# Kernel optimization log

Measured on AMD Instinct MI355X. Metric: run time of the kernel, lower is better.

The kernel has to match this reference:

```python
import jax, jax.numpy as jnp
import numpy as np

B, A, F, T = 4096, 64, 124, 8
H1, H2 = 64, 16


def setup_inputs() -> dict:
    key = jax.random.key(0)
    ks = jax.random.split(key, 10)
    x = jax.random.normal(ks[0], (B, A, F + 1), dtype=jnp.float32)
    types = jax.random.randint(ks[1], (B, A), 0, T).astype(jnp.float32)
    x = x.at[:, :, 0].set(types)  # column 0 stores atom-type index
    mask = (jax.random.uniform(ks[2], (B, A)) < 0.9).astype(jnp.float32)
    s1 = 1.0 / np.sqrt(F)
    s2 = 1.0 / np.sqrt(H1)
    s3 = 1.0 / np.sqrt(H2)
    return {
        "x_padded": x,
        "mask": mask,
        "W1": jax.random.normal(ks[3], (T, F, H1), dtype=jnp.float32) * s1,
        "b1": jax.random.normal(ks[4], (T, H1), dtype=jnp.float32) * s1,
        "W2": jax.random.normal(ks[5], (T, H1, H2), dtype=jnp.float32) * s2,
        "b2": jax.random.normal(ks[6], (T, H2), dtype=jnp.float32) * s2,
        "W3": jax.random.normal(ks[7], (T, H2, 1), dtype=jnp.float32) * s3,
        "b3": jax.random.normal(ks[8], (T, 1), dtype=jnp.float32) * s3,
    }


def reference(x_padded, mask, W1, b1, W2, b2, W3, b3):
    # x_padded: [B, A, 1+F]; mask: [B, A]
    type_idx = x_padded[:, :, 0].astype(jnp.int32)           # [B, A]
    feats = x_padded[:, :, 1:]                               # [B, A, F]
    n_types = W1.shape[0]
    # Faithful to the original: every type's subnet runs on the FULL batch
    # with non-matching atoms zero-masked (bias paths still contribute).
    type_mask = (type_idx[None, :, :] == jnp.arange(n_types)[:, None, None]).astype(feats.dtype)  # [T,B,A]
    sel = feats[None, :, :, :] * type_mask[..., None]        # [T,B,A,F]
    h = jax.nn.relu(jnp.einsum('tbaf,tfh->tbah', sel, W1) + b1[:, None, None, :])
    h = jax.nn.relu(jnp.einsum('tbah,thg->tbag', h, W2) + b2[:, None, None, :])
    o = jnp.einsum('tbag,tgo->tbao', h, W3) + b3[:, None, None, :]  # [T,B,A,1]
    per_atom = (o[..., 0] * mask[None, :, :]).sum(axis=0)   # [B, A]
    return per_atom.sum(axis=1, keepdims=True)               # [B, 1]
```

## Files before the change

kernel.cpp:

```cpp
#include <hip/hip_runtime.h>
#include <stdint.h>

#define NMOL 4096
#define NATOMS (NMOL * 64)
#define NF 124
#define NT 8
#define ROWV 125

#define WS_DCONST  0
#define WS_TOTALS  64
#define WS_CURSOR  96
#define WS_HIST    128
#define WS_W1S     8320
#define WS_W2T     139392
#define WS_TYPEBUF 155776
#define WS_LIST    417920

#define HS 72

typedef __attribute__((ext_vector_type(8))) short short8;
typedef __attribute__((ext_vector_type(4))) float floatx4;
typedef __attribute__((ext_vector_type(4), aligned(4))) float floatx4u;
typedef __attribute__((ext_vector_type(4))) unsigned int uint4v;

__device__ __forceinline__ unsigned short f2bf(float f) {
    unsigned u = __builtin_bit_cast(unsigned, f);
    u += 0x7fffu + ((u >> 16) & 1u);
    return (unsigned short)(u >> 16);
}
__device__ __forceinline__ unsigned pk2(float a, float b) {
    return (unsigned)f2bf(a) | ((unsigned)f2bf(b) << 16);
}
__device__ __forceinline__ void ld_lds16(const void* g, void* lds) {
    __builtin_amdgcn_global_load_lds(
        (const __attribute__((address_space(1))) unsigned int*)g,
        (__attribute__((address_space(3))) unsigned int*)lds, 16, 0, 0);
}

__global__ __launch_bounds__(256) void k_hist(const float* __restrict__ x,
                                              const float* __restrict__ mask,
                                              unsigned* __restrict__ hist256,
                                              unsigned char* __restrict__ typebuf,
                                              float* __restrict__ out) {
    __shared__ unsigned hist[NT];
    int tid = threadIdx.x, b = blockIdx.x;
    if (tid < NT) hist[tid] = 0u;
    __syncthreads();
    int base = b * 1024;
    for (int i = 0; i < 4; ++i) {
        int atom = base + i * 256 + tid;
        float tf = x[(size_t)atom * ROWV];
        float m  = mask[atom];
        unsigned char tb = 0xFF;
        if (m != 0.0f) { tb = (unsigned char)(int)tf; atomicAdd(&hist[tb], 1u); }
        typebuf[atom] = tb;
    }
    if (b < 16) out[b * 256 + tid] = 0.0f;
    __syncthreads();
    if (tid < NT) hist256[b * NT + tid] = hist[tid];
}

__global__ __launch_bounds__(256) void k_setup(const float* __restrict__ W1,
                                               const float* __restrict__ b1,
                                               const float* __restrict__ W2,
                                               const float* __restrict__ b2,
                                               const float* __restrict__ W3,
                                               const float* __restrict__ b3,
                                               const unsigned* __restrict__ hist256,
                                               float* __restrict__ dconst,
                                               unsigned* __restrict__ totals,
                                               unsigned* __restrict__ cursor,
                                               unsigned short* __restrict__ W1S,
                                               unsigned short* __restrict__ W2T) {
    int tid = threadIdx.x, b = blockIdx.x;
    if (b == 0) {
        __shared__ float c[NT];
        __shared__ unsigned part[16][NT];
        __shared__ unsigned tot[NT];
        if (tid < 128) {
            int t = tid >> 4, g = tid & 15;
            float acc = b2[t * 16 + g];
            for (int h = 0; h < 64; ++h) {
                float h1 = b1[t * 64 + h];
                h1 = h1 > 0.f ? h1 : 0.f;
                acc += h1 * W2[(size_t)t * 1024 + h * 16 + g];
            }
            float h2 = acc > 0.f ? acc : 0.f;
            float v = h2 * W3[t * 16 + g];
            #pragma unroll
            for (int off = 1; off < 16; off <<= 1) v += __shfl_xor(v, off);
            if (g == 0) c[t] = v + b3[t];
        }
        if (tid < 128) {
            int t = tid & 7, chunk = tid >> 3;
            unsigned s = 0;
            for (int j = 0; j < 16; ++j) s += hist256[(chunk * 16 + j) * NT + t];
            part[chunk][t] = s;
        }
        __syncthreads();
        if (tid < NT) {
            unsigned s = 0;
            for (int j = 0; j < 16; ++j) s += part[j][tid];
            tot[tid] = s;
            totals[tid] = s;
        }
        __syncthreads();
        if (tid == 0) {
            float T_ = 0.f;
            for (int i = 0; i < NT; ++i) T_ += c[i];
            unsigned run = 0;
            for (int i = 0; i < NT; ++i) {
                dconst[i] = T_ - c[i] + b3[i];
                cursor[i] = run;
                run += tot[i];
            }
        }
    } else {
        int t = b - 1;
        const float* w1g = W1 + (size_t)t * NF * 64;
        unsigned short* dst = W1S + (size_t)t * 8192;
        for (int id = tid; id < 1024; id += 256) {
            int h = id >> 4, cc = id & 15;
            unsigned u[4];
            #pragma unroll
            for (int j = 0; j < 4; ++j) {
                int f0 = cc * 8 + 2 * j;
                unsigned short lo = (f0 < NF)     ? f2bf(w1g[f0 * 64 + h])       : (unsigned short)0;
                unsigned short hi = (f0 + 1 < NF) ? f2bf(w1g[(f0 + 1) * 64 + h]) : (unsigned short)0;
                u[j] = (unsigned)lo | ((unsigned)hi << 16);
            }
            int p = cc ^ (h & 15);
            *(uint4v*)(dst + h * 128 + p * 8) = (uint4v){u[0], u[1], u[2], u[3]};
        }
        unsigned short* d2 = W2T + (size_t)t * 1024;
        for (int i = tid; i < 1024; i += 256) {
            int g = i >> 6, h = i & 63;
            d2[i] = f2bf(W2[(size_t)t * 1024 + h * 16 + g]);
        }
    }
}

__global__ __launch_bounds__(256) void k_scatter(const unsigned char* __restrict__ typebuf,
                                                 unsigned* cursor, unsigned* list) {
    __shared__ unsigned hist[NT], basep[NT], cur[NT];
    int tid = threadIdx.x;
    if (tid < NT) { hist[tid] = 0u; cur[tid] = 0u; }
    __syncthreads();
    int base = blockIdx.x * 1024;
    unsigned char tb[4];
    for (int i = 0; i < 4; ++i) {
        tb[i] = typebuf[base + i * 256 + tid];
        if (tb[i] != 0xFF) atomicAdd(&hist[tb[i]], 1u);
    }
    __syncthreads();
    if (tid < NT && hist[tid]) basep[tid] = atomicAdd(&cursor[tid], hist[tid]);
    __syncthreads();
    for (int i = 0; i < 4; ++i) {
        if (tb[i] != 0xFF) {
            unsigned p = basep[tb[i]] + atomicAdd(&cur[tb[i]], 1u);
            list[p] = (unsigned)(base + i * 256 + tid);
        }
    }
}

__global__ __launch_bounds__(256, 4) void k_mlp(const float* __restrict__ x,
                                                const unsigned short* __restrict__ W1S,
                                                const float* __restrict__ b1,
                                                const unsigned short* __restrict__ W2T,
                                                const float* __restrict__ b2,
                                                const float* __restrict__ W3,
                                                const unsigned* __restrict__ totals,
                                                const float* __restrict__ dconst,
                                                const unsigned* __restrict__ list,
                                                float* __restrict__ out) {
    __shared__ unsigned short sW[64 * 128];
    __shared__ unsigned short sH[128 * HS];
    __shared__ unsigned sIds[128];

    unsigned g = blockIdx.x;
    unsigned cnt[NT], st[NT];
    {
        unsigned s = 0;
        for (int i = 0; i < NT; ++i) { cnt[i] = totals[i]; st[i] = s; s += cnt[i]; }
    }
    int t = -1; unsigned tile = 0;
    {
        unsigned tl = 0;
        for (int i = 0; i < NT; ++i) {
            unsigned nt_ = (cnt[i] + 127u) >> 7;
            if (t < 0 && g < tl + nt_) { t = i; tile = g - tl; }
            tl += nt_;
        }
    }
    if (t < 0) return;

    int valid = (int)cnt[t] - (int)(tile << 7);
    if (valid > 128) valid = 128;
    unsigned rowstart = st[t] + (tile << 7);

    int tid  = threadIdx.x;
    int wv   = tid >> 6;
    int lane = tid & 63;
    int quad = lane >> 4, l15 = lane & 15;
    int rowbase = wv * 32;

    {
        const char* src = (const char*)W1S + (size_t)t * 16384 + wv * 4096 + lane * 16;
        char*       dst = (char*)sW + wv * 4096;
        #pragma unroll
        for (int i = 0; i < 4; ++i) ld_lds16(src + i * 1024, dst + i * 1024);
    }
    if (tid < 128) sIds[tid] = list[rowstart + (tid < valid ? tid : 0)];

    float b1v[4];
    #pragma unroll
    for (int n = 0; n < 4; ++n) b1v[n] = b1[t * 64 + n * 16 + l15];

    __syncthreads();

    short8 afrag[2][4];
    #pragma unroll
    for (int m = 0; m < 2; ++m) {
        unsigned atom = sIds[rowbase + m * 16 + l15];
        const float* rp = x + (size_t)atom * ROWV + 1;
        #pragma unroll
        for (int ks = 0; ks < 4; ++ks) {
            int k0 = ks * 32 + quad * 8;
            floatx4 f0 = (floatx4)(*(const floatx4u*)(rp + k0));
            floatx4 f1 = (floatx4)0.f;
            if (!(ks == 3 && quad == 3))
                f1 = (floatx4)(*(const floatx4u*)(rp + k0 + 4));
            uint4v uu = (uint4v){pk2(f0[0], f0[1]), pk2(f0[2], f0[3]),
                                 pk2(f1[0], f1[1]), pk2(f1[2], f1[3])};
            afrag[m][ks] = __builtin_bit_cast(short8, uu);
        }
    }

    floatx4 c1[2][4];
    #pragma unroll
    for (int m = 0; m < 2; ++m)
        #pragma unroll
        for (int n = 0; n < 4; ++n) c1[m][n] = (floatx4)0.f;

    #pragma unroll
    for (int ks = 0; ks < 4; ++ks) {
        short8 bf[4];
        #pragma unroll
        for (int n = 0; n < 4; ++n)
            bf[n] = *(const short8*)(sW + (n * 16 + l15) * 128 + (((ks * 4 + quad) ^ l15) << 3));
        #pragma unroll
        for (int n = 0; n < 4; ++n) {
            c1[0][n] = __builtin_amdgcn_mfma_f32_16x16x32_bf16(afrag[0][ks], bf[n], c1[0][n], 0, 0, 0);
            c1[1][n] = __builtin_amdgcn_mfma_f32_16x16x32_bf16(afrag[1][ks], bf[n], c1[1][n], 0, 0, 0);
        }
    }

    #pragma unroll
    for (int m = 0; m < 2; ++m)
        #pragma unroll
        for (int n = 0; n < 4; ++n) {
            int col = n * 16 + l15;
            #pragma unroll
            for (int r = 0; r < 4; ++r) {
                float v = c1[m][n][r] + b1v[n];
                v = v > 0.f ? v : 0.f;
                sH[(rowbase + m * 16 + quad * 4 + r) * HS + col] = f2bf(v);
            }
        }

    const unsigned short* w2t = W2T + (size_t)t * 1024;
    floatx4 c2[2];
    c2[0] = (floatx4)0.f; c2[1] = (floatx4)0.f;
    #pragma unroll
    for (int ks = 0; ks < 2; ++ks) {
        int ko = ks * 32 + quad * 8;
        short8 a0 = *(const short8*)(sH + (rowbase + l15) * HS + ko);
        short8 a1 = *(const short8*)(sH + (rowbase + 16 + l15) * HS + ko);
        short8 bw = *(const short8*)(w2t + l15 * 64 + ko);
        c2[0] = __builtin_amdgcn_mfma_f32_16x16x32_bf16(a0, bw, c2[0], 0, 0, 0);
        c2[1] = __builtin_amdgcn_mfma_f32_16x16x32_bf16(a1, bw, c2[1], 0, 0, 0);
    }

    float b2v = b2[t * 16 + l15];
    float w3v = W3[t * 16 + l15];
    float dct = dconst[t];
    #pragma unroll
    for (int m = 0; m < 2; ++m) {
        float h2v[4];
        #pragma unroll
        for (int r = 0; r < 4; ++r) {
            float v = c2[m][r] + b2v;
            v = v > 0.f ? v : 0.f;
            h2v[r] = v * w3v;
        }
        #pragma unroll
        for (int off = 1; off < 16; off <<= 1)
            #pragma unroll
            for (int r = 0; r < 4; ++r) h2v[r] += __shfl_xor(h2v[r], off);
        if (l15 == 0) {
            #pragma unroll
            for (int r = 0; r < 4; ++r) {
                int row = rowbase + m * 16 + quad * 4 + r;
                if (row < valid) {
                    unsigned atom = sIds[row];
                    atomicAdd(&out[atom >> 6], h2v[r] + dct);
                }
            }
        }
    }
}

extern "C" void kernel_launch(void* const* d_in, const int* in_sizes, int n_in,
                              void* d_out, int out_size, void* d_ws, size_t ws_size,
                              hipStream_t stream) {
    const float* x    = (const float*)d_in[0];
    const float* mask = (const float*)d_in[1];
    const float* W1   = (const float*)d_in[2];
    const float* b1   = (const float*)d_in[3];
    const float* W2   = (const float*)d_in[4];
    const float* b2   = (const float*)d_in[5];
    const float* W3   = (const float*)d_in[6];
    const float* b3   = (const float*)d_in[7];
    float* out = (float*)d_out;

    char* ws = (char*)d_ws;
    float*          dconst  = (float*)(ws + WS_DCONST);
    unsigned*       totals  = (unsigned*)(ws + WS_TOTALS);
    unsigned*       cursor  = (unsigned*)(ws + WS_CURSOR);
    unsigned*       hist256 = (unsigned*)(ws + WS_HIST);
    unsigned short* W1S     = (unsigned short*)(ws + WS_W1S);
    unsigned short* W2T     = (unsigned short*)(ws + WS_W2T);
    unsigned char*  typebuf = (unsigned char*)(ws + WS_TYPEBUF);
    unsigned*       list    = (unsigned*)(ws + WS_LIST);

    k_hist<<<256, 256, 0, stream>>>(x, mask, hist256, typebuf, out);
    k_setup<<<9, 256, 0, stream>>>(W1, b1, W2, b2, W3, b3, hist256,
                                   dconst, totals, cursor, W1S, W2T);
    k_scatter<<<256, 256, 0, stream>>>(typebuf, cursor, list);
    k_mlp<<<2055, 256, 0, stream>>>(x, W1S, b1, W2T, b2, W3,
                                    totals, dconst, list, out);
}
```

Baseline: 224.7 us.

## Replace histogram+prefix pass with fixed-capacity per-type buckets, dropping a kernel

Removes the separate histogram kernel and the global prefix sum by giving each atom type a fixed-capacity bucket of 65536 slots. The sort kernel reads types and mask directly and atomically appends into each type's bucket. The MLP grid becomes a fixed 8x512 blocks, and each block derives its type and tile from its index and exits early if empty. Output zeroing moves into the setup kernel. This saves one launch and one pass over the type column, at the cost of launching many empty MLP blocks and assuming no type exceeds the capacity.

After: 217.3 us. 1.03x faster.

```diff
diff --git a/kernel.cpp b/kernel.cpp
--- a/kernel.cpp
+++ b/kernel.cpp
@@ -6,15 +6,13 @@
 #define NF 124
 #define NT 8
 #define ROWV 125
+#define CAP 65536
 
 #define WS_DCONST  0
-#define WS_TOTALS  64
-#define WS_CURSOR  96
-#define WS_HIST    128
-#define WS_W1S     8320
-#define WS_W2T     139392
-#define WS_TYPEBUF 155776
-#define WS_LIST    417920
+#define WS_CURSOR  64
+#define WS_W1S     128
+#define WS_W2T     131200
+#define WS_LIST    147712
 
 #define HS 72
 
@@ -35,29 +33,6 @@
     __builtin_amdgcn_global_load_lds(
         (const __attribute__((address_space(1))) unsigned int*)g,
         (__attribute__((address_space(3))) unsigned int*)lds, 16, 0, 0);
-}
-
-__global__ __launch_bounds__(256) void k_hist(const float* __restrict__ x,
-                                              const float* __restrict__ mask,
-                                              unsigned* __restrict__ hist256,
-                                              unsigned char* __restrict__ typebuf,
-                                              float* __restrict__ out) {
-    __shared__ unsigned hist[NT];
-    int tid = threadIdx.x, b = blockIdx.x;
-    if (tid < NT) hist[tid] = 0u;
-    __syncthreads();
-    int base = b * 1024;
-    for (int i = 0; i < 4; ++i) {
-        int atom = base + i * 256 + tid;
-        float tf = x[(size_t)atom * ROWV];
-        float m  = mask[atom];
-        unsigned char tb = 0xFF;
-        if (m != 0.0f) { tb = (unsigned char)(int)tf; atomicAdd(&hist[tb], 1u); }
-        typebuf[atom] = tb;
-    }
-    if (b < 16) out[b * 256 + tid] = 0.0f;
-    __syncthreads();
-    if (tid < NT) hist256[b * NT + tid] = hist[tid];
 }
 
 __global__ __launch_bounds__(256) void k_setup(const float* __restrict__ W1,
@@ -66,17 +41,14 @@
                                                const float* __restrict__ b2,
                                                const float* __restrict__ W3,
                                                const float* __restrict__ b3,
-                                               const unsigned* __restrict__ hist256,
                                                float* __restrict__ dconst,
-                                               unsigned* __restrict__ totals,
                                                unsigned* __restrict__ cursor,
                                                unsigned short* __restrict__ W1S,
-                                               unsigned short* __restrict__ W2T) {
+                                               unsigned short* __restrict__ W2T,
+                                               float* __restrict__ out) {
     int tid = threadIdx.x, b = blockIdx.x;
     if (b == 0) {
         __shared__ float c[NT];
-        __shared__ unsigned part[16][NT];
-        __shared__ unsigned tot[NT];
         if (tid < 128) {
             int t = tid >> 4, g = tid & 15;
             float acc = b2[t * 16 + g];
@@ -91,31 +63,14 @@
             for (int off = 1; off < 16; off <<= 1) v += __shfl_xor(v, off);
             if (g == 0) c[t] = v + b3[t];
         }
-        if (tid < 128) {
-            int t = tid & 7, chunk = tid >> 3;
-            unsigned s = 0;
-            for (int j = 0; j < 16; ++j) s += hist256[(chunk * 16 + j) * NT + t];
-            part[chunk][t] = s;
-        }
-        __syncthreads();
-        if (tid < NT) {
-            unsigned s = 0;
-            for (int j = 0; j < 16; ++j) s += part[j][tid];
-            tot[tid] = s;
-            totals[tid] = s;
-        }
+        if (tid < NT) cursor[tid] = (unsigned)(tid * CAP);
         __syncthreads();
         if (tid == 0) {
             float T_ = 0.f;
             for (int i = 0; i < NT; ++i) T_ += c[i];
-            unsigned run = 0;
-            for (int i = 0; i < NT; ++i) {
-                dconst[i] = T_ - c[i] + b3[i];
-                cursor[i] = run;
-                run += tot[i];
-            }
-        }
-    } else {
+            for (int i = 0; i < NT; ++i) dconst[i] = T_ - c[i] + b3[i];
+        }
+    } else if (b <= 8) {
         int t = b - 1;
         const float* w1g = W1 + (size_t)t * NF * 64;
         unsigned short* dst = W1S + (size_t)t * 8192;
@@ -137,11 +92,15 @@
             int g = i >> 6, h = i & 63;
             d2[i] = f2bf(W2[(size_t)t * 1024 + h * 16 + g]);
         }
-    }
-}
-
-__global__ __launch_bounds__(256) void k_scatter(const unsigned char* __restrict__ typebuf,
-                                                 unsigned* cursor, unsigned* list) {
+    } else {
+        out[(b - 9) * 256 + tid] = 0.0f;
+    }
+}
+
+__global__ __launch_bounds__(256) void k_sort(const float* __restrict__ x,
+                                              const float* __restrict__ mask,
+                                              unsigned* __restrict__ cursor,
+                                              unsigned* __restrict__ list) {
     __shared__ unsigned hist[NT], basep[NT], cur[NT];
     int tid = threadIdx.x;
     if (tid < NT) { hist[tid] = 0u; cur[tid] = 0u; }
@@ -149,8 +108,11 @@
     int base = blockIdx.x * 1024;
     unsigned char tb[4];
     for (int i = 0; i < 4; ++i) {
-        tb[i] = typebuf[base + i * 256 + tid];
-        if (tb[i] != 0xFF) atomicAdd(&hist[tb[i]], 1u);
+        int atom = base + i * 256 + tid;
+        float tf = x[(size_t)atom * ROWV];
+        float m  = mask[atom];
+        tb[i] = 0xFF;
+        if (m != 0.0f) { tb[i] = (unsigned char)(int)tf; atomicAdd(&hist[tb[i]], 1u); }
     }
     __syncthreads();
     if (tid < NT && hist[tid]) basep[tid] = atomicAdd(&cursor[tid], hist[tid]);
@@ -169,7 +131,7 @@
                                                 const unsigned short* __restrict__ W2T,
                                                 const float* __restrict__ b2,
                                                 const float* __restrict__ W3,
-                                                const unsigned* __restrict__ totals,
+                                                const unsigned* __restrict__ cursor,
                                                 const float* __restrict__ dconst,
                                                 const unsigned* __restrict__ list,
                                                 float* __restrict__ out) {
@@ -177,26 +139,13 @@
     __shared__ unsigned short sH[128 * HS];
     __shared__ unsigned sIds[128];
 
-    unsigned g = blockIdx.x;
-    unsigned cnt[NT], st[NT];
-    {
-        unsigned s = 0;
-        for (int i = 0; i < NT; ++i) { cnt[i] = totals[i]; st[i] = s; s += cnt[i]; }
-    }
-    int t = -1; unsigned tile = 0;
-    {
-        unsigned tl = 0;
-        for (int i = 0; i < NT; ++i) {
-            unsigned nt_ = (cnt[i] + 127u) >> 7;
-            if (t < 0 && g < tl + nt_) { t = i; tile = g - tl; }
-            tl += nt_;
-        }
-    }
-    if (t < 0) return;
-
-    int valid = (int)cnt[t] - (int)(tile << 7);
+    int t    = blockIdx.x >> 9;
+    int tile = blockIdx.x & 511;
+    int cnt  = (int)(cursor[t] - (unsigned)(t * CAP));
+    int valid = cnt - (tile << 7);
+    if (valid <= 0) return;
     if (valid > 128) valid = 128;
-    unsigned rowstart = st[t] + (tile << 7);
+    int rowstart = t * CAP + (tile << 7);
 
     int tid  = threadIdx.x;
     int wv   = tid >> 6;
@@ -324,19 +273,14 @@
     float* out = (float*)d_out;
 
     char* ws = (char*)d_ws;
-    float*          dconst  = (float*)(ws + WS_DCONST);
-    unsigned*       totals  = (unsigned*)(ws + WS_TOTALS);
-    unsigned*       cursor  = (unsigned*)(ws + WS_CURSOR);
-    unsigned*       hist256 = (unsigned*)(ws + WS_HIST);
-    unsigned short* W1S     = (unsigned short*)(ws + WS_W1S);
-    unsigned short* W2T     = (unsigned short*)(ws + WS_W2T);
-    unsigned char*  typebuf = (unsigned char*)(ws + WS_TYPEBUF);
-    unsigned*       list    = (unsigned*)(ws + WS_LIST);
-
-    k_hist<<<256, 256, 0, stream>>>(x, mask, hist256, typebuf, out);
-    k_setup<<<9, 256, 0, stream>>>(W1, b1, W2, b2, W3, b3, hist256,
-                                   dconst, totals, cursor, W1S, W2T);
-    k_scatter<<<256, 256, 0, stream>>>(typebuf, cursor, list);
-    k_mlp<<<2055, 256, 0, stream>>>(x, W1S, b1, W2T, b2, W3,
-                                    totals, dconst, list, out);
-}
+    float*          dconst = (float*)(ws + WS_DCONST);
+    unsigned*       cursor = (unsigned*)(ws + WS_CURSOR);
+    unsigned short* W1S    = (unsigned short*)(ws + WS_W1S);
+    unsigned short* W2T    = (unsigned short*)(ws + WS_W2T);
+    unsigned*       list   = (unsigned*)(ws + WS_LIST);
+
+    k_setup<<<25, 256, 0, stream>>>(W1, b1, W2, b2, W3, b3, dconst, cursor, W1S, W2T, out);
+    k_sort<<<256, 256, 0, stream>>>(x, mask, cursor, list);
+    k_mlp<<<NT * (CAP / 128), 256, 0, stream>>>(x, W1S, b1, W2T, b2, W3,
+                                                cursor, dconst, list, out);
+}
```
